# Optimization experiments

Hardware: AMD Instinct MI355X
Metric: run time of the kernel (lower is better)

## Reference

```python
import jax, jax.numpy as jnp
import numpy as np

HIDDEN = 512
N_STEPS = 24
BATCH = 64
SEQ = 512
LN_EPS = 1e-5


def setup_inputs() -> dict:
    key = jax.random.key(0)
    ks = jax.random.split(key, 12)
    h = HIDDEN
    s = 0.05
    return {
        "enc_outputs": jax.random.normal(ks[0], (BATCH, SEQ, h), jnp.float32),
        "h_prev": jax.random.normal(ks[1], (1, BATCH, h), jnp.float32),
        # additive attention: score = v^T tanh(W_a [dec; enc] + b_a)
        "attn_We": jax.random.normal(ks[2], (h, h), jnp.float32) * s,   # enc half of W_a
        "attn_Wd": jax.random.normal(ks[3], (h, h), jnp.float32) * s,   # dec half of W_a
        "attn_b": jnp.zeros((h,), jnp.float32),
        "attn_v": jax.random.normal(ks[4], (h,), jnp.float32) * s,
        # GRU (PyTorch layout): W_ih (3h, 2h), W_hh (3h, h), gate order r,z,n
        "W_ih": jax.random.normal(ks[5], (3 * h, 2 * h), jnp.float32) * s,
        "W_hh": jax.random.normal(ks[6], (3 * h, h), jnp.float32) * s,
        "b_ih": jnp.zeros((3 * h,), jnp.float32),
        "b_hh": jnp.zeros((3 * h,), jnp.float32),
        # head: LayerNorm -> Linear(h, h//2) -> ReLU -> Linear(h//2, 1)
        "ln_g": jnp.ones((h,), jnp.float32),
        "ln_b": jnp.zeros((h,), jnp.float32),
        "W1": jax.random.normal(ks[7], (h, h // 2), jnp.float32) * s,
        "b1": jnp.zeros((h // 2,), jnp.float32),
        "W2": jax.random.normal(ks[8], (h // 2, 1), jnp.float32) * s,
        "b2": jnp.zeros((1,), jnp.float32),
    }


def _decode(enc_outputs, h0, attn_We, attn_Wd, attn_b, attn_v,
            W_ih, W_hh, b_ih, b_hh, ln_g, ln_b, W1, b1, W2, b2):
    H = enc_outputs.shape[-1]
    # encoder projection is loop-invariant: precompute once
    enc_proj = jnp.einsum("bse,eh->bsh", enc_outputs, attn_We)  # (B,S,H)

    def step(h, _):
        # h: (B, H) decoder state
        # additive attention
        q = h @ attn_Wd + attn_b                                  # (B,H)
        scores = jnp.einsum("bsh,h->bs", jnp.tanh(enc_proj + q[:, None, :]), attn_v)
        alpha = jax.nn.softmax(scores, axis=-1)                   # (B,S)
        context = jnp.einsum("bs,bsh->bh", alpha, enc_outputs)   # (B,H)
        # GRU cell on [context; state]
        x = jnp.concatenate([context, h], axis=-1)                # (B,2H)
        gi = x @ W_ih.T + b_ih                                    # (B,3H)
        gh = h @ W_hh.T + b_hh                                    # (B,3H)
        ir, iz, inn = jnp.split(gi, 3, axis=-1)
        hr, hz, hn = jnp.split(gh, 3, axis=-1)
        r = jax.nn.sigmoid(ir + hr)
        z = jax.nn.sigmoid(iz + hz)
        n = jnp.tanh(inn + r * hn)
        h_new = (1.0 - z) * n + z * h
        # head: LN -> Linear -> ReLU -> Linear
        mu = jnp.mean(h_new, axis=-1, keepdims=True)
        var = jnp.var(h_new, axis=-1, keepdims=True)
        y = (h_new - mu) * jax.lax.rsqrt(var + LN_EPS) * ln_g + ln_b
        y = jax.nn.relu(y @ W1 + b1)
        p = (y @ W2 + b2)[:, 0]                                   # (B,)
        return h_new, p

    h_final, preds = jax.lax.scan(step, h0, None, length=N_STEPS)
    preds = jnp.transpose(preds, (1, 0))[:, :, None]              # (B, n_steps, 1)
    return preds, h_final[None]                                   # (1,B,H)


def reference(enc_outputs, h_prev, attn_We, attn_Wd, attn_b, attn_v,
              W_ih, W_hh, b_ih, b_hh, ln_g, ln_b, W1, b1, W2, b2):
    return _decode(enc_outputs, h_prev[0], attn_We, attn_Wd, attn_b, attn_v,
                   W_ih, W_hh, b_ih, b_hh, ln_g, ln_b, W1, b1, W2, b2)
```

## Files before the change

kernel.cpp:

```cpp
#include <hip/hip_runtime.h>

typedef unsigned short u16;
typedef __attribute__((ext_vector_type(8))) short short8;
typedef __attribute__((ext_vector_type(4))) short short4v;
typedef __attribute__((ext_vector_type(4))) float f32x4;

#define NSTEP 24

__device__ __forceinline__ float b2f(u16 u){ return __uint_as_float(((unsigned)u)<<16); }
__device__ __forceinline__ u16 f2b(float f){
  unsigned u = __float_as_uint(f);
  u += 0x7fffu + ((u>>16)&1u);
  return (u16)(u>>16);
}
__device__ __forceinline__ float tanh_fast(float x){
  x = fminf(12.f, fmaxf(-12.f, x));
  float e = __expf(2.f*x);
  return __fdividef(e-1.f, e+1.f);
}
__device__ __forceinline__ float sigmoid_fast(float x){
  return __fdividef(1.f, 1.f + __expf(-x));
}

__global__ __launch_bounds__(256) void k_cvt(const float* __restrict__ in, u16* __restrict__ out, int n){
  int i = (blockIdx.x*256 + threadIdx.x)*4;
  if (i >= n) return;
  float4 v = *(const float4*)(in + i);
  short4v o;
  o[0] = (short)f2b(v.x); o[1] = (short)f2b(v.y); o[2] = (short)f2b(v.z); o[3] = (short)f2b(v.w);
  *(short4v*)(out + i) = o;
}

__global__ __launch_bounds__(256) void k_transpose512(const float* __restrict__ in, u16* __restrict__ out){
  __shared__ float tile[32][33];
  int tx = threadIdx.x, ty = threadIdx.y;
  int x = blockIdx.x*32 + tx;
  #pragma unroll
  for (int j=0;j<4;++j){
    int y = blockIdx.y*32 + ty + j*8;
    tile[ty+j*8][tx] = in[y*512 + x];
  }
  __syncthreads();
  int x2 = blockIdx.y*32 + tx;
  #pragma unroll
  for (int j=0;j<4;++j){
    int y2 = blockIdx.x*32 + ty + j*8;
    out[y2*512 + x2] = f2b(tile[tx][ty+j*8]);
  }
}

__global__ __launch_bounds__(256) void k_init(const float* __restrict__ h0, float* __restrict__ hf, u16* __restrict__ xcat){
  int idx = blockIdx.x*256 + threadIdx.x;
  float v = h0[idx];
  hf[idx] = v;
  xcat[(idx>>9)*1024 + 512 + (idx&511)] = f2b(v);
}

__global__ __launch_bounds__(256) void k_encproj(const u16* __restrict__ A, const u16* __restrict__ BT, u16* __restrict__ C){
  int w = threadIdx.x>>6, lane = threadIdx.x&63;
  int m0 = blockIdx.x*128 + (w>>1)*64;
  int n0 = blockIdx.y*128 + (w&1)*64;
  int r16 = lane&15, kof = (lane>>4)<<3;
  const u16* Ap = A + (m0+r16)*512 + kof;
  const u16* Bp = BT + (n0+r16)*512 + kof;
  f32x4 acc[4][4];
  #pragma unroll
  for (int i=0;i<4;++i)
    #pragma unroll
    for (int j=0;j<4;++j) acc[i][j] = (f32x4){0.f,0.f,0.f,0.f};
  for (int k0=0;k0<512;k0+=32){
    short8 a[4], b[4];
    #pragma unroll
    for (int mf=0;mf<4;++mf) a[mf] = *(const short8*)(Ap + mf*16*512 + k0);
    #pragma unroll
    for (int nf=0;nf<4;++nf) b[nf] = *(const short8*)(Bp + nf*16*512 + k0);
    #pragma unroll
    for (int mf=0;mf<4;++mf)
      #pragma unroll
      for (int nf=0;nf<4;++nf)
        acc[mf][nf] = __builtin_amdgcn_mfma_f32_16x16x32_bf16(a[mf], b[nf], acc[mf][nf], 0,0,0);
  }
  int rb = (lane>>4)<<2;
  #pragma unroll
  for (int mf=0;mf<4;++mf)
    #pragma unroll
    for (int nf=0;nf<4;++nf)
      #pragma unroll
      for (int r=0;r<4;++r)
        C[(m0+mf*16+rb+r)*512 + n0+nf*16+r16] = f2b(acc[mf][nf][r]);
}

__device__ __forceinline__ void gemm_bt_core(const u16* A, int lda, const u16* BT, int ldb,
    const float* bias, float* C, int ldc, int K, int widx){
  int lane = threadIdx.x & 63;
  int mt = widx & 3, nt = widx >> 2;
  int m0 = mt<<4, n0 = nt<<6;
  int r16 = lane&15, kof = (lane>>4)<<3;
  const u16* Ap = A + (m0+r16)*lda + kof;
  const u16* Bp = BT + (n0+r16)*ldb + kof;
  f32x4 acc[4];
  #pragma unroll
  for (int i=0;i<4;++i) acc[i] = (f32x4){0.f,0.f,0.f,0.f};
  for (int k0=0;k0<K;k0+=32){
    short8 a = *(const short8*)(Ap + k0);
    #pragma unroll
    for (int nf=0;nf<4;++nf){
      short8 b = *(const short8*)(Bp + nf*16*ldb + k0);
      acc[nf] = __builtin_amdgcn_mfma_f32_16x16x32_bf16(a, b, acc[nf], 0,0,0);
    }
  }
  int rb = (lane>>4)<<2;
  #pragma unroll
  for (int nf=0;nf<4;++nf){
    int col = n0 + nf*16 + r16;
    float bv = bias[col];
    #pragma unroll
    for (int r=0;r<4;++r)
      C[(m0+rb+r)*ldc + col] = acc[nf][r] + bv;
  }
}

__global__ __launch_bounds__(256) void k_gru_gemm(const u16* __restrict__ xcat,
    const u16* __restrict__ Wih, const float* __restrict__ bih,
    const u16* __restrict__ Whh, const float* __restrict__ bhh,
    float* __restrict__ gi, float* __restrict__ gh){
  int widx = blockIdx.x*4 + (threadIdx.x>>6);
  if (blockIdx.y == 0)
    gemm_bt_core(xcat,       1024, Wih, 1024, bih, gi, 1536, 1024, widx);
  else
    gemm_bt_core(xcat + 512, 1024, Whh,  512, bhh, gh, 1536,  512, widx);
}

__device__ __forceinline__ void q_core(const float* hl, const u16* WdT, const float* ab, float* qrow){
  int tid = threadIdx.x;
  #pragma unroll
  for (int jj=0;jj<2;++jj){
    int j = tid + jj*256;
    float acc = ab[j];
    const u16* wr = WdT + j*512;
    #pragma unroll 4
    for (int k0=0;k0<512;k0+=8){
      short8 wv = *(const short8*)(wr + k0);
      #pragma unroll
      for (int i=0;i<8;++i) acc = fmaf(hl[k0+i], b2f((u16)wv[i]), acc);
    }
    qrow[j] = acc;
  }
}

__global__ __launch_bounds__(256) void k_q0(const float* __restrict__ hf, const u16* __restrict__ WdT,
    const float* __restrict__ ab, float* __restrict__ q){
  __shared__ float hl[512];
  int t = threadIdx.x, b = blockIdx.x;
  hl[t] = hf[b*512 + t];
  hl[t+256] = hf[b*512 + 256 + t];
  __syncthreads();
  q_core(hl, WdT, ab, q + b*512);
}

__global__ __launch_bounds__(256) void k_score(const u16* __restrict__ ep, const float* __restrict__ q,
    const float* __restrict__ av, float* __restrict__ sc){
  __shared__ float qs[512], vs[512];
  int t = threadIdx.x, b = blockIdx.y;
  qs[t]     = q[b*512 + t];
  qs[t+256] = q[b*512 + 256 + t];
  vs[t]     = av[t];
  vs[t+256] = av[256 + t];
  __syncthreads();
  int w = t>>6, lane = t&63;
  float qv[8], vv[8];
  #pragma unroll
  for (int j=0;j<8;++j){ qv[j] = qs[lane*8+j]; vv[j] = vs[lane*8+j]; }
  int s0 = blockIdx.x*16 + w*4;
  #pragma unroll
  for (int i=0;i<4;++i){
    int s = s0 + i;
    short8 e = *(const short8*)(ep + (b*512+s)*512 + lane*8);
    float acc = 0.f;
    #pragma unroll
    for (int j=0;j<8;++j)
      acc += vv[j]*tanh_fast(b2f((u16)e[j]) + qv[j]);
    #pragma unroll
    for (int off=32; off; off>>=1) acc += __shfl_xor(acc, off);
    if (lane==0) sc[b*512 + s] = acc;
  }
}

__global__ __launch_bounds__(512) void k_softctx(const float* __restrict__ sc, const u16* __restrict__ encB,
    u16* __restrict__ xcat){
  __shared__ float red[512];
  __shared__ float al[512];
  __shared__ float part[8][512];
  int t = threadIdx.x, b = blockIdx.x;
  float s1 = sc[b*512 + t];
  red[t] = s1; __syncthreads();
  for (int off=256; off; off>>=1){ if (t<off) red[t] = fmaxf(red[t], red[t+off]); __syncthreads(); }
  float mx = red[0]; __syncthreads();
  float e1 = __expf(s1-mx);
  red[t] = e1; __syncthreads();
  for (int off=256; off; off>>=1){ if (t<off) red[t] += red[t+off]; __syncthreads(); }
  float inv = __fdividef(1.f, red[0]);
  al[t] = e1*inv;
  __syncthreads();
  int lane = t&63, w = t>>6;
  int hg = lane*8;
  float a8[8];
  #pragma unroll
  for (int j=0;j<8;++j) a8[j] = 0.f;
  const u16* eb = encB + (b*512 + w*64)*512 + hg;
  const float* alp = al + w*64;
  for (int s=0;s<64;++s){
    short8 e = *(const short8*)(eb + s*512);
    float a = alp[s];
    #pragma unroll
    for (int j=0;j<8;++j) a8[j] = fmaf(a, b2f((u16)e[j]), a8[j]);
  }
  #pragma unroll
  for (int j=0;j<8;++j) part[w][hg+j] = a8[j];
  __syncthreads();
  float v = 0.f;
  #pragma unroll
  for (int w2=0;w2<8;++w2) v += part[w2][t];
  xcat[b*1024 + t] = f2b(v);
}

__global__ __launch_bounds__(256) void k_fin(const float* __restrict__ gi, const float* __restrict__ gh,
    const float* __restrict__ lng, const float* __restrict__ lnb,
    const float* __restrict__ W1, const float* __restrict__ b1,
    const float* __restrict__ W2, const float* __restrict__ b2,
    const u16* __restrict__ WdT, const float* __restrict__ ab,
    float* __restrict__ hf, u16* __restrict__ xcat, float* __restrict__ q,
    float* __restrict__ out, int step){
  __shared__ float hl[512];
  __shared__ float yn[512];
  __shared__ float red[256];
  int tid = threadIdx.x, b = blockIdx.x;
  #pragma unroll
  for (int jj=0;jj<2;++jj){
    int n = tid + jj*256;
    int gb = b*1536 + n;
    float r  = sigmoid_fast(gi[gb]      + gh[gb]);
    float z  = sigmoid_fast(gi[gb+512]  + gh[gb+512]);
    float nn = tanh_fast(gi[gb+1024] + r*gh[gb+1024]);
    float hp = hf[b*512 + n];
    float hnew = (1.f-z)*nn + z*hp;
    hf[b*512 + n] = hnew;
    xcat[b*1024 + 512 + n] = f2b(hnew);
    hl[n] = hnew;
    if (step == NSTEP-1) out[1536 + b*512 + n] = hnew;
  }
  __syncthreads();
  float h1 = hl[tid], h2 = hl[tid+256];
  red[tid] = h1+h2; __syncthreads();
  for (int off=128; off; off>>=1){ if (tid<off) red[tid]+=red[tid+off]; __syncthreads(); }
  float mu = red[0]*(1.f/512.f); __syncthreads();
  red[tid] = h1*h1+h2*h2; __syncthreads();
  for (int off=128; off; off>>=1){ if (tid<off) red[tid]+=red[tid+off]; __syncthreads(); }
  float var = red[0]*(1.f/512.f) - mu*mu; __syncthreads();
  float rs = rsqrtf(var + 1e-5f);
  yn[tid]     = (h1-mu)*rs*lng[tid] + lnb[tid];
  yn[tid+256] = (h2-mu)*rs*lng[tid+256] + lnb[tid+256];
  __syncthreads();
  float acc = b1[tid];
  #pragma unroll 8
  for (int k=0;k<512;++k) acc = fmaf(yn[k], W1[k*256+tid], acc);
  float y = fmaxf(acc, 0.f);
  red[tid] = y*W2[tid]; __syncthreads();
  for (int off=128; off; off>>=1){ if (tid<off) red[tid]+=red[tid+off]; __syncthreads(); }
  if (tid==0) out[b*24 + step] = red[0] + b2[0];
  if (step < NSTEP-1){
    __syncthreads();
    q_core(hl, WdT, ab, q + b*512);
  }
}

extern "C" void kernel_launch(void* const* d_in, const int* in_sizes, int n_in,
                              void* d_out, int out_size, void* d_ws, size_t ws_size,
                              hipStream_t stream){
  (void)in_sizes; (void)n_in; (void)out_size; (void)ws_size;
  const float* enc = (const float*)d_in[0];
  const float* h0  = (const float*)d_in[1];
  const float* We  = (const float*)d_in[2];
  const float* Wd  = (const float*)d_in[3];
  const float* ab  = (const float*)d_in[4];
  const float* av  = (const float*)d_in[5];
  const float* Wih = (const float*)d_in[6];
  const float* Whh = (const float*)d_in[7];
  const float* bih = (const float*)d_in[8];
  const float* bhh = (const float*)d_in[9];
  const float* lng = (const float*)d_in[10];
  const float* lnb = (const float*)d_in[11];
  const float* W1  = (const float*)d_in[12];
  const float* b1  = (const float*)d_in[13];
  const float* W2  = (const float*)d_in[14];
  const float* b2  = (const float*)d_in[15];
  float* out = (float*)d_out;
  char* ws = (char*)d_ws;
  u16*  ep   = (u16*)(ws + 0);
  u16*  encB = (u16*)(ws + 33554432);
  u16*  WeT  = (u16*)(ws + 67108864);
  u16*  WdT  = (u16*)(ws + 67633152);
  u16*  WihB = (u16*)(ws + 68157440);
  u16*  WhhB = (u16*)(ws + 71303168);
  float* hf  = (float*)(ws + 72876032);
  u16*  xcat = (u16*)(ws + 73007104);
  float* q   = (float*)(ws + 73138176);
  float* sc  = (float*)(ws + 73269248);
  float* gi  = (float*)(ws + 73400320);
  float* gh  = (float*)(ws + 73793536);

  k_cvt<<<16384, 256, 0, stream>>>(enc, encB, 16777216);
  k_cvt<<<1536, 256, 0, stream>>>(Wih, WihB, 1572864);
  k_cvt<<<768, 256, 0, stream>>>(Whh, WhhB, 786432);
  k_transpose512<<<dim3(16,16), dim3(32,8), 0, stream>>>(We, WeT);
  k_transpose512<<<dim3(16,16), dim3(32,8), 0, stream>>>(Wd, WdT);
  k_init<<<128, 256, 0, stream>>>(h0, hf, xcat);
  k_encproj<<<dim3(256,4), 256, 0, stream>>>(encB, WeT, ep);
  k_q0<<<64, 256, 0, stream>>>(hf, WdT, ab, q);
  for (int t=0; t<NSTEP; ++t){
    k_score<<<dim3(32,64), 256, 0, stream>>>(ep, q, av, sc);
    k_softctx<<<64, 512, 0, stream>>>(sc, encB, xcat);
    k_gru_gemm<<<dim3(24,2), 256, 0, stream>>>(xcat, WihB, bih, WhhB, bhh, gi, gh);
    k_fin<<<64, 256, 0, stream>>>(gi, gh, lng, lnb, W1, b1, W2, b2, WdT, ab,
                                  hf, xcat, q, out, t);
  }
}
```

Measured before the change: 2.164 ms.

## Overlap hidden-state GRU GEMMs with attention scoring and split context over more blocks

The h-dependent GRU GEMMs (W_hh and the h half of W_ih) now run inside the scoring kernel as extra blocks, since they do not depend on the context. The context half of W_ih runs afterwards in its own kernel and accumulates into gi. Softmax plus context is split across 4 hidden-chunk blocks per batch, giving 256 blocks instead of 64, at the cost of recomputing the softmax in each block. The score loop keeps four row loads in flight at once, and some GEMM loops get unroll pragmas. This adds a read-modify-write of gi and an extra launch in exchange for more parallelism and overlap.

```diff
diff --git a/kernel.cpp b/kernel.cpp
--- a/kernel.cpp
+++ b/kernel.cpp
@@ -68,6 +68,7 @@
   for (int i=0;i<4;++i)
     #pragma unroll
     for (int j=0;j<4;++j) acc[i][j] = (f32x4){0.f,0.f,0.f,0.f};
+  #pragma unroll
   for (int k0=0;k0<512;k0+=32){
     short8 a[4], b[4];
     #pragma unroll
@@ -91,7 +92,7 @@
 }
 
 __device__ __forceinline__ void gemm_bt_core(const u16* A, int lda, const u16* BT, int ldb,
-    const float* bias, float* C, int ldc, int K, int widx){
+    const float* bias, float* C, int ldc, int K, int widx, bool accum){
   int lane = threadIdx.x & 63;
   int mt = widx & 3, nt = widx >> 2;
   int m0 = mt<<4, n0 = nt<<6;
@@ -101,6 +102,7 @@
   f32x4 acc[4];
   #pragma unroll
   for (int i=0;i<4;++i) acc[i] = (f32x4){0.f,0.f,0.f,0.f};
+  #pragma unroll 4
   for (int k0=0;k0<K;k0+=32){
     short8 a = *(const short8*)(Ap + k0);
     #pragma unroll
@@ -113,22 +115,115 @@
   #pragma unroll
   for (int nf=0;nf<4;++nf){
     int col = n0 + nf*16 + r16;
-    float bv = bias[col];
-    #pragma unroll
-    for (int r=0;r<4;++r)
-      C[(m0+rb+r)*ldc + col] = acc[nf][r] + bv;
-  }
-}
-
-__global__ __launch_bounds__(256) void k_gru_gemm(const u16* __restrict__ xcat,
-    const u16* __restrict__ Wih, const float* __restrict__ bih,
-    const u16* __restrict__ Whh, const float* __restrict__ bhh,
-    float* __restrict__ gi, float* __restrict__ gh){
+    float bv = bias ? bias[col] : 0.f;
+    #pragma unroll
+    for (int r=0;r<4;++r){
+      float* p = &C[(m0+rb+r)*ldc + col];
+      float v = acc[nf][r] + bv;
+      if (accum) v += *p;
+      *p = v;
+    }
+  }
+}
+
+__global__ __launch_bounds__(256) void k_sgh(const u16* __restrict__ ep, const float* __restrict__ q,
+    const float* __restrict__ av, const u16* __restrict__ xcat,
+    const u16* __restrict__ WhhB, const float* __restrict__ bhh,
+    const u16* __restrict__ WihB, const float* __restrict__ bih,
+    float* __restrict__ sc, float* __restrict__ gh, float* __restrict__ gi){
+  int bid = blockIdx.x, tid = threadIdx.x;
+  int wid = tid>>6, lane = tid&63;
+  if (bid < 2048){
+    int b = bid >> 5, sq = bid & 31;
+    float qv[8], vv[8];
+    {
+      float4 q0 = *(const float4*)(q + b*512 + lane*8);
+      float4 q1 = *(const float4*)(q + b*512 + lane*8 + 4);
+      qv[0]=q0.x; qv[1]=q0.y; qv[2]=q0.z; qv[3]=q0.w;
+      qv[4]=q1.x; qv[5]=q1.y; qv[6]=q1.z; qv[7]=q1.w;
+      float4 v0 = *(const float4*)(av + lane*8);
+      float4 v1 = *(const float4*)(av + lane*8 + 4);
+      vv[0]=v0.x; vv[1]=v0.y; vv[2]=v0.z; vv[3]=v0.w;
+      vv[4]=v1.x; vv[5]=v1.y; vv[6]=v1.z; vv[7]=v1.w;
+    }
+    int srow = sq*16 + wid*4;
+    const u16* base = ep + (b*512 + srow)*512 + lane*8;
+    short8 e0 = *(const short8*)(base);
+    short8 e1 = *(const short8*)(base + 512);
+    short8 e2 = *(const short8*)(base + 1024);
+    short8 e3 = *(const short8*)(base + 1536);
+    float r0=0.f, r1=0.f, r2=0.f, r3=0.f;
+    #pragma unroll
+    for (int j=0;j<8;++j){
+      r0 += vv[j]*tanh_fast(b2f((u16)e0[j]) + qv[j]);
+      r1 += vv[j]*tanh_fast(b2f((u16)e1[j]) + qv[j]);
+      r2 += vv[j]*tanh_fast(b2f((u16)e2[j]) + qv[j]);
+      r3 += vv[j]*tanh_fast(b2f((u16)e3[j]) + qv[j]);
+    }
+    #pragma unroll
+    for (int off=32; off; off>>=1){
+      r0 += __shfl_xor(r0, off);
+      r1 += __shfl_xor(r1, off);
+      r2 += __shfl_xor(r2, off);
+      r3 += __shfl_xor(r3, off);
+    }
+    if (lane==0){
+      sc[b*512 + srow]   = r0;
+      sc[b*512 + srow+1] = r1;
+      sc[b*512 + srow+2] = r2;
+      sc[b*512 + srow+3] = r3;
+    }
+  } else if (bid < 2072){
+    gemm_bt_core(xcat+512, 1024, WhhB, 512, bhh, gh, 1536, 512, (bid-2048)*4 + wid, false);
+  } else {
+    gemm_bt_core(xcat+512, 1024, WihB+512, 1024, bih, gi, 1536, 512, (bid-2072)*4 + wid, false);
+  }
+}
+
+__global__ __launch_bounds__(256) void k_ctx(const float* __restrict__ sc, const u16* __restrict__ encB,
+    u16* __restrict__ xcat){
+  __shared__ float red[256];
+  __shared__ float al[512];
+  __shared__ float part[16][128];
+  int t = threadIdx.x, hc = blockIdx.x, b = blockIdx.y;
+  float s1 = sc[b*512 + t], s2 = sc[b*512 + 256 + t];
+  red[t] = fmaxf(s1, s2); __syncthreads();
+  for (int off=128; off; off>>=1){ if (t<off) red[t] = fmaxf(red[t], red[t+off]); __syncthreads(); }
+  float mx = red[0]; __syncthreads();
+  float e1 = __expf(s1-mx), e2 = __expf(s2-mx);
+  red[t] = e1+e2; __syncthreads();
+  for (int off=128; off; off>>=1){ if (t<off) red[t] += red[t+off]; __syncthreads(); }
+  float inv = __fdividef(1.f, red[0]);
+  al[t] = e1*inv; al[t+256] = e2*inv;
+  __syncthreads();
+  int cg = t & 15, sg = t >> 4;
+  const u16* eb = encB + (b*512 + sg*32)*512 + hc*128 + cg*8;
+  const float* alp = al + sg*32;
+  float a8[8];
+  #pragma unroll
+  for (int j=0;j<8;++j) a8[j] = 0.f;
+  #pragma unroll 8
+  for (int s=0;s<32;++s){
+    short8 e = *(const short8*)(eb + s*512);
+    float a = alp[s];
+    #pragma unroll
+    for (int j=0;j<8;++j) a8[j] = fmaf(a, b2f((u16)e[j]), a8[j]);
+  }
+  #pragma unroll
+  for (int j=0;j<8;++j) part[sg][cg*8+j] = a8[j];
+  __syncthreads();
+  if (t < 128){
+    float v = 0.f;
+    #pragma unroll
+    for (int sg2=0;sg2<16;++sg2) v += part[sg2][t];
+    xcat[b*1024 + hc*128 + t] = f2b(v);
+  }
+}
+
+__global__ __launch_bounds__(256) void k_gictx(const u16* __restrict__ xcat, const u16* __restrict__ WihB,
+    float* __restrict__ gi){
   int widx = blockIdx.x*4 + (threadIdx.x>>6);
-  if (blockIdx.y == 0)
-    gemm_bt_core(xcat,       1024, Wih, 1024, bih, gi, 1536, 1024, widx);
-  else
-    gemm_bt_core(xcat + 512, 1024, Whh,  512, bhh, gh, 1536,  512, widx);
+  gemm_bt_core(xcat, 1024, WihB, 1024, (const float*)0, gi, 1536, 512, widx, true);
 }
 
 __device__ __forceinline__ void q_core(const float* hl, const u16* WdT, const float* ab, float* qrow){
@@ -156,72 +251,6 @@
   hl[t+256] = hf[b*512 + 256 + t];
   __syncthreads();
   q_core(hl, WdT, ab, q + b*512);
-}
-
-__global__ __launch_bounds__(256) void k_score(const u16* __restrict__ ep, const float* __restrict__ q,
-    const float* __restrict__ av, float* __restrict__ sc){
-  __shared__ float qs[512], vs[512];
-  int t = threadIdx.x, b = blockIdx.y;
-  qs[t]     = q[b*512 + t];
-  qs[t+256] = q[b*512 + 256 + t];
-  vs[t]     = av[t];
-  vs[t+256] = av[256 + t];
-  __syncthreads();
-  int w = t>>6, lane = t&63;
-  float qv[8], vv[8];
-  #pragma unroll
-  for (int j=0;j<8;++j){ qv[j] = qs[lane*8+j]; vv[j] = vs[lane*8+j]; }
-  int s0 = blockIdx.x*16 + w*4;
-  #pragma unroll
-  for (int i=0;i<4;++i){
-    int s = s0 + i;
-    short8 e = *(const short8*)(ep + (b*512+s)*512 + lane*8);
-    float acc = 0.f;
-    #pragma unroll
-    for (int j=0;j<8;++j)
-      acc += vv[j]*tanh_fast(b2f((u16)e[j]) + qv[j]);
-    #pragma unroll
-    for (int off=32; off; off>>=1) acc += __shfl_xor(acc, off);
-    if (lane==0) sc[b*512 + s] = acc;
-  }
-}
-
-__global__ __launch_bounds__(512) void k_softctx(const float* __restrict__ sc, const u16* __restrict__ encB,
-    u16* __restrict__ xcat){
-  __shared__ float red[512];
-  __shared__ float al[512];
-  __shared__ float part[8][512];
-  int t = threadIdx.x, b = blockIdx.x;
-  float s1 = sc[b*512 + t];
-  red[t] = s1; __syncthreads();
-  for (int off=256; off; off>>=1){ if (t<off) red[t] = fmaxf(red[t], red[t+off]); __syncthreads(); }
-  float mx = red[0]; __syncthreads();
-  float e1 = __expf(s1-mx);
-  red[t] = e1; __syncthreads();
-  for (int off=256; off; off>>=1){ if (t<off) red[t] += red[t+off]; __syncthreads(); }
-  float inv = __fdividef(1.f, red[0]);
-  al[t] = e1*inv;
-  __syncthreads();
-  int lane = t&63, w = t>>6;
-  int hg = lane*8;
-  float a8[8];
-  #pragma unroll
-  for (int j=0;j<8;++j) a8[j] = 0.f;
-  const u16* eb = encB + (b*512 + w*64)*512 + hg;
-  const float* alp = al + w*64;
-  for (int s=0;s<64;++s){
-    short8 e = *(const short8*)(eb + s*512);
-    float a = alp[s];
-    #pragma unroll
-    for (int j=0;j<8;++j) a8[j] = fmaf(a, b2f((u16)e[j]), a8[j]);
-  }
-  #pragma unroll
-  for (int j=0;j<8;++j) part[w][hg+j] = a8[j];
-  __syncthreads();
-  float v = 0.f;
-  #pragma unroll
-  for (int w2=0;w2<8;++w2) v += part[w2][t];
-  xcat[b*1024 + t] = f2b(v);
 }
 
 __global__ __launch_bounds__(256) void k_fin(const float* __restrict__ gi, const float* __restrict__ gh,
@@ -318,9 +347,9 @@
   k_encproj<<<dim3(256,4), 256, 0, stream>>>(encB, WeT, ep);
   k_q0<<<64, 256, 0, stream>>>(hf, WdT, ab, q);
   for (int t=0; t<NSTEP; ++t){
-    k_score<<<dim3(32,64), 256, 0, stream>>>(ep, q, av, sc);
-    k_softctx<<<64, 512, 0, stream>>>(sc, encB, xcat);
-    k_gru_gemm<<<dim3(24,2), 256, 0, stream>>>(xcat, WihB, bih, WhhB, bhh, gi, gh);
+    k_sgh<<<2096, 256, 0, stream>>>(ep, q, av, xcat, WhhB, bhh, WihB, bih, sc, gh, gi);
+    k_ctx<<<dim3(4,64), 256, 0, stream>>>(sc, encB, xcat);
+    k_gictx<<<24, 256, 0, stream>>>(xcat, WihB, gi);
     k_fin<<<64, 256, 0, stream>>>(gi, gh, lng, lnb, W1, b1, W2, b2, WdT, ab,
                                   hf, xcat, q, out, t);
   }
```

Result: slower. 2.255 ms (+4.2%).
